# Performance work log

Measured on AMD Instinct MI355X. Metric: run time of the kernel, lower is better.

## Reference

```python
import jax, jax.numpy as jnp
import numpy as np

N = 50000
E = 400000
IN_DIM = 256
HID = 64
HEADS = 8
OUT_DIM = 40
NEG_SLOPE = 0.2  # PyG GATConv leaky-relu slope


def gat_conv(x, src, dst, W, a_src, a_dst, bias, concat):
    """One PyG-style GATConv (eval mode, self-loops already appended).
    x: [N, in], W: [in, H*C], a_src/a_dst: [H, C], bias: [H*C] or [C]."""
    H, C = a_src.shape
    h = (x @ W).reshape(N, H, C)                       # [N, H, C]
    # per-node attention logits, gathered per edge
    e_src = (h * a_src[None]).sum(-1)                  # [N, H]
    e_dst = (h * a_dst[None]).sum(-1)                  # [N, H]
    alpha = jax.nn.leaky_relu(e_src[src] + e_dst[dst], NEG_SLOPE)  # [Etot, H]
    # segment softmax over incoming edges of each dst node
    amax = jax.ops.segment_max(alpha, dst, num_segments=N)         # [N, H]
    ex = jnp.exp(alpha - amax[dst])
    denom = jax.ops.segment_sum(ex, dst, num_segments=N)           # [N, H]
    coef = ex / denom[dst]                                         # [Etot, H]
    # weighted scatter-add of neighbor features
    msg = h[src] * coef[:, :, None]                                # [Etot, H, C]
    out = jax.ops.segment_sum(msg, dst, num_segments=N)            # [N, H, C]
    out = out.reshape(N, H * C) if concat else out.mean(axis=1)
    return out + bias


def setup_inputs() -> dict:
    key = jax.random.key(0)
    ks = jax.random.split(key, 10)
    x = jax.random.normal(ks[0], (N, IN_DIM), dtype=jnp.float32)
    edge_index = jax.random.randint(ks[1], (2, E), 0, N, dtype=jnp.int32)
    g1 = 1.0 / np.sqrt(IN_DIM)
    g2 = 1.0 / np.sqrt(HID * HEADS)
    W1 = jax.random.normal(ks[2], (IN_DIM, HEADS * HID), dtype=jnp.float32) * g1
    a_src1 = jax.random.normal(ks[3], (HEADS, HID), dtype=jnp.float32) * 0.1
    a_dst1 = jax.random.normal(ks[4], (HEADS, HID), dtype=jnp.float32) * 0.1
    b1 = jnp.zeros((HEADS * HID,), dtype=jnp.float32)
    W2 = jax.random.normal(ks[5], (HEADS * HID, OUT_DIM), dtype=jnp.float32) * g2
    a_src2 = jax.random.normal(ks[6], (1, OUT_DIM), dtype=jnp.float32) * 0.1
    a_dst2 = jax.random.normal(ks[7], (1, OUT_DIM), dtype=jnp.float32) * 0.1
    b2 = jnp.zeros((OUT_DIM,), dtype=jnp.float32)
    return {"x": x, "edge_index": edge_index, "W1": W1, "a_src1": a_src1,
            "a_dst1": a_dst1, "b1": b1, "W2": W2, "a_src2": a_src2,
            "a_dst2": a_dst2, "b2": b2}


def reference(x, edge_index, W1, a_src1, a_dst1, b1, W2, a_src2, a_dst2, b2):
    # append self loops (PyG GATConv default add_self_loops=True)
    loop = jnp.arange(N, dtype=edge_index.dtype)
    src = jnp.concatenate([edge_index[0], loop])
    dst = jnp.concatenate([edge_index[1], loop])
    h = gat_conv(x, src, dst, W1, a_src1, a_dst1, b1, concat=True)
    h = jax.nn.elu(h)
    # dropout is identity in eval mode
    out = gat_conv(h, src, dst, W2, a_src2, a_dst2, b2, concat=False)
    return out
```

## Files before the change

kernel.cpp:

```cpp
#include <hip/hip_runtime.h>
#include <hip/hip_bf16.h>
#include <math.h>

#define IN_DIM 256
#define HEADS 8
#define HID 64
#define HC1 512
#define OUT_DIM 40
#define NEG_SLOPE 0.2f

typedef __attribute__((ext_vector_type(8))) short short8;
typedef __attribute__((ext_vector_type(4))) float f32x4;

__device__ __forceinline__ unsigned short f2b(float f) {
    __hip_bfloat16 h = __float2bfloat16(f);
    unsigned short u;
    __builtin_memcpy(&u, &h, 2);
    return u;
}

#define LRELU(a) ((a) > 0.f ? (a) : NEG_SLOPE * (a))

#define NB_W ((HC1 * IN_DIM + 48 * HC1 + 255) / 256)

__global__ __launch_bounds__(256) void prologue_kernel(
    const float* __restrict__ W1, const float* __restrict__ W2,
    __hip_bfloat16* __restrict__ W1T, __hip_bfloat16* __restrict__ W2T,
    const int* __restrict__ ei, int* __restrict__ deg, int E, int ET)
{
    int b = blockIdx.x;
    if (b < NB_W) {
        int i = b * 256 + threadIdx.x;
        if (i < HC1 * IN_DIM) {
            int n = i >> 8, k = i & 255;
            W1T[i] = __float2bfloat16(W1[(size_t)k * HC1 + n]);
        }
        int j = i - HC1 * IN_DIM;
        if (j >= 0 && j < 48 * HC1) {
            int n = j >> 9, k = j & 511;
            W2T[j] = __float2bfloat16(n < OUT_DIM ? W2[(size_t)k * OUT_DIM + n] : 0.f);
        }
    } else {
        int e = (b - NB_W) * 256 + threadIdx.x;
        if (e >= ET) return;
        int d = (e < E) ? ei[E + e] : e - E;
        atomicAdd(&deg[d], 1);
    }
}


__global__ __launch_bounds__(256) void scan1_kernel(
    const int* __restrict__ deg, int* __restrict__ rowptr,
    int* __restrict__ aux, int N)
{
    __shared__ int sd[256];
    int tid = threadIdx.x;
    int i = blockIdx.x * 256 + tid;
    int v = (i < N) ? deg[i] : 0;
    sd[tid] = v;
    __syncthreads();
    for (int off = 1; off < 256; off <<= 1) {
        int t = (tid >= off) ? sd[tid - off] : 0;
        __syncthreads();
        sd[tid] += t;
        __syncthreads();
    }
    if (i < N) rowptr[i] = sd[tid] - v;
    if (tid == 255) aux[blockIdx.x] = sd[255];
}

__global__ __launch_bounds__(256) void scan_aux_kernel(int* __restrict__ aux, int nb)
{
    __shared__ int sd[256];
    int tid = threadIdx.x;
    int v = (tid < nb) ? aux[tid] : 0;
    sd[tid] = v;
    __syncthreads();
    for (int off = 1; off < 256; off <<= 1) {
        int t = (tid >= off) ? sd[tid - off] : 0;
        __syncthreads();
        sd[tid] += t;
        __syncthreads();
    }
    if (tid < nb) aux[tid] = sd[tid] - v;
}

__global__ __launch_bounds__(256) void scan_add_kernel(
    int* __restrict__ rowptr, int* __restrict__ cursor,
    const int* __restrict__ aux, int N, int ET)
{
    int i = blockIdx.x * 256 + threadIdx.x;
    if (i < N) {
        int v = rowptr[i] + aux[blockIdx.x];
        rowptr[i] = v;
        cursor[i] = v;
    }
    if (i == 0) rowptr[N] = ET;
}

__global__ __launch_bounds__(256) void build_kernel(
    const int* __restrict__ ei, int* __restrict__ cursor,
    int* __restrict__ csr_src, int E, int ET)
{
    int e = blockIdx.x * 256 + threadIdx.x;
    if (e >= ET) return;
    int s, d;
    if (e < E) { s = ei[e]; d = ei[E + e]; } else { s = d = e - E; }
    int pos = atomicAdd(&cursor[d], 1);
    csr_src[pos] = s;
}

__global__ __launch_bounds__(512) void gemm1_mfma(
    const float* __restrict__ x, const __hip_bfloat16* __restrict__ W1T,
    const float* __restrict__ a_src1, const float* __restrict__ a_dst1,
    __hip_bfloat16* __restrict__ h1, float* __restrict__ e_src1,
    float* __restrict__ e_dst1, int N)
{
    __shared__ __hip_bfloat16 As[64][264];
    const int tid = threadIdx.x;
    const int row0 = blockIdx.x * 64;

    {
        int rr = tid >> 3;
        int cb = (tid & 7) * 32;
        int rowc = row0 + rr; if (rowc >= N) rowc = N - 1;
        const float* xp = x + (size_t)rowc * IN_DIM + cb;
#pragma unroll
        for (int j = 0; j < 4; ++j) {
            float4 a0 = *(const float4*)(xp + 8 * j);
            float4 a1 = *(const float4*)(xp + 8 * j + 4);
            short8 v;
            v[0] = f2b(a0.x); v[1] = f2b(a0.y); v[2] = f2b(a0.z); v[3] = f2b(a0.w);
            v[4] = f2b(a1.x); v[5] = f2b(a1.y); v[6] = f2b(a1.z); v[7] = f2b(a1.w);
            *(short8*)(&As[rr][cb + 8 * j]) = v;
        }
    }
    __syncthreads();

    const int w = tid >> 6;
    const int lane = tid & 63;
    const int r = lane & 15, g = lane >> 4;

    f32x4 acc[4][4] = {};
    const short* bp = (const short*)W1T + (size_t)(w * 64 + r) * IN_DIM + 8 * g;

#pragma unroll 2
    for (int kk = 0; kk < IN_DIM; kk += 32) {
        short8 af[4];
#pragma unroll
        for (int rt = 0; rt < 4; ++rt)
            af[rt] = *(const short8*)(&As[rt * 16 + r][kk + 8 * g]);
        short8 bf[4];
#pragma unroll
        for (int t = 0; t < 4; ++t)
            bf[t] = *(const short8*)(bp + (size_t)t * 16 * IN_DIM + kk);
#pragma unroll
        for (int t = 0; t < 4; ++t)
#pragma unroll
            for (int rt = 0; rt < 4; ++rt)
                acc[rt][t] = __builtin_amdgcn_mfma_f32_16x16x32_bf16(
                    af[rt], bf[t], acc[rt][t], 0, 0, 0);
    }

#pragma unroll
    for (int rt = 0; rt < 4; ++rt)
#pragma unroll
        for (int t = 0; t < 4; ++t) {
            int c = w * 64 + t * 16 + r;
#pragma unroll
            for (int q = 0; q < 4; ++q) {
                int row = row0 + rt * 16 + 4 * g + q;
                if (row < N)
                    h1[(size_t)row * HC1 + c] = __float2bfloat16(acc[rt][t][q]);
            }
        }

    float a1v[4], a2v[4];
#pragma unroll
    for (int t = 0; t < 4; ++t) {
        a1v[t] = a_src1[w * 64 + t * 16 + r];
        a2v[t] = a_dst1[w * 64 + t * 16 + r];
    }
#pragma unroll
    for (int rt = 0; rt < 4; ++rt) {
        float ps[4] = {}, pd[4] = {};
#pragma unroll
        for (int t = 0; t < 4; ++t)
#pragma unroll
            for (int q = 0; q < 4; ++q) {
                ps[q] += acc[rt][t][q] * a1v[t];
                pd[q] += acc[rt][t][q] * a2v[t];
            }
#pragma unroll
        for (int off = 1; off < 16; off <<= 1)
#pragma unroll
            for (int q = 0; q < 4; ++q) {
                ps[q] += __shfl_xor(ps[q], off);
                pd[q] += __shfl_xor(pd[q], off);
            }
        if (r == 0) {
#pragma unroll
            for (int q = 0; q < 4; ++q) {
                int row = row0 + rt * 16 + 4 * g + q;
                if (row < N) {
                    e_src1[row * 8 + w] = ps[q];
                    e_dst1[row * 8 + w] = pd[q];
                }
            }
        }
    }
}

__global__ __launch_bounds__(256) void gather1_kernel(
    const int* __restrict__ rowptr, const int* __restrict__ csr_src,
    const __hip_bfloat16* __restrict__ h1, const float* __restrict__ e_src,
    const float* __restrict__ e_dst, const float* __restrict__ b1,
    __hip_bfloat16* __restrict__ hmid, int N)
{
    int d = blockIdx.x * 4 + (threadIdx.x >> 6);
    if (d >= N) return;
    const int lane = threadIdx.x & 63;
    const int h0 = lane >> 3;
    const int base = rowptr[d];
    const int deg = rowptr[d + 1] - base;
    const float edv = e_dst[d * 8 + (lane & 7)];

    float acc[8] = {};
    float ssum = 0.f;

    const int nch = (deg + 7) >> 3;
    for (int c = 0; c < nch; ++c) {
        int i = c * 8 + (lane >> 3);
        int ii = i < deg ? i : deg - 1;
        int s = csr_src[base + ii];
        float v = e_src[s * 8 + (lane & 7)] + edv;
        float coef = (i < deg) ? __expf(LRELU(v)) : 0.f;

        uint4 u[8];
        float ce[8];
#pragma unroll
        for (int e = 0; e < 8; ++e) {
            ce[e] = __shfl(coef, e * 8 + h0);
            int se = __shfl(s, e * 8);
            u[e] = *(const uint4*)(h1 + (size_t)se * HC1 + 8 * lane);
        }
#pragma unroll
        for (int e = 0; e < 8; ++e) {
            acc[0] += ce[e] * __uint_as_float(u[e].x << 16);
            acc[1] += ce[e] * __uint_as_float(u[e].x & 0xffff0000u);
            acc[2] += ce[e] * __uint_as_float(u[e].y << 16);
            acc[3] += ce[e] * __uint_as_float(u[e].y & 0xffff0000u);
            acc[4] += ce[e] * __uint_as_float(u[e].z << 16);
            acc[5] += ce[e] * __uint_as_float(u[e].z & 0xffff0000u);
            acc[6] += ce[e] * __uint_as_float(u[e].w << 16);
            acc[7] += ce[e] * __uint_as_float(u[e].w & 0xffff0000u);
            ssum += ce[e];
        }
    }

    float inv = 1.f / ssum;
    float4 b0 = *(const float4*)(b1 + 8 * lane);
    float4 b4 = *(const float4*)(b1 + 8 * lane + 4);
    float ob[8];
    ob[0] = acc[0] * inv + b0.x; ob[1] = acc[1] * inv + b0.y;
    ob[2] = acc[2] * inv + b0.z; ob[3] = acc[3] * inv + b0.w;
    ob[4] = acc[4] * inv + b4.x; ob[5] = acc[5] * inv + b4.y;
    ob[6] = acc[6] * inv + b4.z; ob[7] = acc[7] * inv + b4.w;
    unsigned short rr[8];
#pragma unroll
    for (int j = 0; j < 8; ++j) {
        float o = ob[j];
        o = o > 0.f ? o : expm1f(o);
        rr[j] = f2b(o);
    }
    *(uint4*)(hmid + (size_t)d * HC1 + 8 * lane) = *(uint4*)rr;
}

__global__ __launch_bounds__(256) void gemm2_mfma(
    const __hip_bfloat16* __restrict__ hmid, const __hip_bfloat16* __restrict__ W2T,
    const float* __restrict__ a_src2, const float* __restrict__ a_dst2,
    float* __restrict__ h2, float* __restrict__ e_src2, float* __restrict__ e_dst2,
    int N)
{
    __shared__ __hip_bfloat16 Bs[48][520];
    const int tid = threadIdx.x;

    {
        const short* wp = (const short*)W2T;
#pragma unroll
        for (int i = 0; i < 12; ++i) {
            int idx = tid + i * 256;
            int row = idx >> 6, ch = idx & 63;
            *(short8*)(&Bs[row][ch * 8]) = *(const short8*)(wp + (size_t)row * HC1 + ch * 8);
        }
    }
    __syncthreads();

    const int w = tid >> 6;
    const int lane = tid & 63;
    const int r = lane & 15, g = lane >> 4;
    const int rowW = blockIdx.x * 64 + w * 16;

    int arow = rowW + r; if (arow >= N) arow = N - 1;
    const short* ap = (const short*)hmid + (size_t)arow * HC1 + 8 * g;

    f32x4 acc[3] = {};
#pragma unroll 4
    for (int kk = 0; kk < HC1; kk += 32) {
        short8 af = *(const short8*)(ap + kk);
        short8 bf[3];
#pragma unroll
        for (int t = 0; t < 3; ++t)
            bf[t] = *(const short8*)(&Bs[t * 16 + r][kk + 8 * g]);
#pragma unroll
        for (int t = 0; t < 3; ++t)
            acc[t] = __builtin_amdgcn_mfma_f32_16x16x32_bf16(af, bf[t], acc[t], 0, 0, 0);
    }

#pragma unroll
    for (int t = 0; t < 3; ++t) {
        int c = t * 16 + r;
        if (c < OUT_DIM) {
#pragma unroll
            for (int q = 0; q < 4; ++q) {
                int row = rowW + 4 * g + q;
                if (row < N) h2[(size_t)row * OUT_DIM + c] = acc[t][q];
            }
        }
    }

    float as[3], ad[3];
#pragma unroll
    for (int t = 0; t < 3; ++t) {
        int c = t * 16 + r;
        as[t] = (c < OUT_DIM) ? a_src2[c] : 0.f;
        ad[t] = (c < OUT_DIM) ? a_dst2[c] : 0.f;
    }
    float ps[4] = {}, pd[4] = {};
#pragma unroll
    for (int t = 0; t < 3; ++t)
#pragma unroll
        for (int q = 0; q < 4; ++q) {
            ps[q] += acc[t][q] * as[t];
            pd[q] += acc[t][q] * ad[t];
        }
#pragma unroll
    for (int off = 1; off < 16; off <<= 1)
#pragma unroll
        for (int q = 0; q < 4; ++q) {
            ps[q] += __shfl_xor(ps[q], off);
            pd[q] += __shfl_xor(pd[q], off);
        }
    if (r == 0) {
#pragma unroll
        for (int q = 0; q < 4; ++q) {
            int row = rowW + 4 * g + q;
            if (row < N) { e_src2[row] = ps[q]; e_dst2[row] = pd[q]; }
        }
    }
}

__global__ __launch_bounds__(256) void gather2_kernel(
    const int* __restrict__ rowptr, const int* __restrict__ csr_src,
    const float* __restrict__ h2, const float* __restrict__ e_src,
    const float* __restrict__ e_dst, const float* __restrict__ b2,
    float* __restrict__ out, int N)
{
    int wid = (blockIdx.x * blockDim.x + threadIdx.x) >> 6;
    if (wid >= N) return;
    int lane = threadIdx.x & 63;
    int base = rowptr[wid], end = rowptr[wid + 1];
    float ed = e_dst[wid];
    bool act = lane < OUT_DIM;
    int ln = act ? lane : 0;

    float acc = 0.f, ssum = 0.f;
    int j = base;
    for (; j + 4 <= end; j += 4) {
        int s0 = csr_src[j], s1 = csr_src[j + 1], s2 = csr_src[j + 2], s3 = csr_src[j + 3];
        float v0 = e_src[s0] + ed, v1 = e_src[s1] + ed;
        float v2 = e_src[s2] + ed, v3 = e_src[s3] + ed;
        float f0 = h2[(size_t)s0 * OUT_DIM + ln];
        float f1 = h2[(size_t)s1 * OUT_DIM + ln];
        float f2 = h2[(size_t)s2 * OUT_DIM + ln];
        float f3 = h2[(size_t)s3 * OUT_DIM + ln];
        float e0 = __expf(LRELU(v0)), e1 = __expf(LRELU(v1));
        float e2 = __expf(LRELU(v2)), e3 = __expf(LRELU(v3));
        acc += e0 * f0 + e1 * f1 + e2 * f2 + e3 * f3;
        ssum += e0 + e1 + e2 + e3;
    }
    for (; j < end; ++j) {
        int s0 = csr_src[j];
        float v0 = e_src[s0] + ed;
        float f0 = h2[(size_t)s0 * OUT_DIM + ln];
        float e0 = __expf(LRELU(v0));
        acc += e0 * f0;
        ssum += e0;
    }
    if (act)
        out[(size_t)wid * OUT_DIM + lane] = acc / ssum + b2[lane];
}

extern "C" void kernel_launch(void* const* d_in, const int* in_sizes, int n_in,
                              void* d_out, int out_size, void* d_ws, size_t ws_size,
                              hipStream_t stream)
{
    const float* x      = (const float*)d_in[0];
    const int*   ei     = (const int*)d_in[1];
    const float* W1     = (const float*)d_in[2];
    const float* a_src1 = (const float*)d_in[3];
    const float* a_dst1 = (const float*)d_in[4];
    const float* b1     = (const float*)d_in[5];
    const float* W2     = (const float*)d_in[6];
    const float* a_src2 = (const float*)d_in[7];
    const float* a_dst2 = (const float*)d_in[8];
    const float* b2     = (const float*)d_in[9];
    float* out = (float*)d_out;

    const int N  = in_sizes[0] / IN_DIM;
    const int E  = in_sizes[1] / 2;
    const int ET = E + N;

    char* p = (char*)d_ws;
    auto alloc = [&](size_t bytes) -> void* {
        void* r = (void*)p;
        p += (bytes + 255) & ~(size_t)255;
        return r;
    };
    __hip_bfloat16* h1b    = (__hip_bfloat16*)alloc((size_t)N * HC1 * 2);
    __hip_bfloat16* hmid   = (__hip_bfloat16*)alloc((size_t)N * HC1 * 2);
    float*    h2      = (float*)alloc((size_t)N * OUT_DIM * 4);
    float*    e_src1  = (float*)alloc((size_t)N * HEADS * 4);
    float*    e_dst1  = (float*)alloc((size_t)N * HEADS * 4);
    float*    e_src2  = (float*)alloc((size_t)N * 4);
    float*    e_dst2  = (float*)alloc((size_t)N * 4);
    int*      deg     = (int*)alloc((size_t)N * 4);
    int*      rowptr  = (int*)alloc((size_t)(N + 1) * 4);
    int*      cursor  = (int*)alloc((size_t)N * 4);
    int*      csr_src = (int*)alloc((size_t)ET * 4);
    int*      aux     = (int*)alloc(256 * 4);
    __hip_bfloat16* W1T = (__hip_bfloat16*)alloc((size_t)HC1 * IN_DIM * 2);
    __hip_bfloat16* W2T = (__hip_bfloat16*)alloc((size_t)48 * HC1 * 2);

    const int nbN  = (N + 255) / 256;
    const int nbET = (ET + 255) / 256;

    hipMemsetAsync(deg, 0, (size_t)N * 4, stream);
    prologue_kernel<<<NB_W + nbET, 256, 0, stream>>>(W1, W2, W1T, W2T, ei, deg, E, ET);

    scan1_kernel<<<nbN, 256, 0, stream>>>(deg, rowptr, aux, N);
    scan_aux_kernel<<<1, 256, 0, stream>>>(aux, nbN);
    scan_add_kernel<<<nbN, 256, 0, stream>>>(rowptr, cursor, aux, N, ET);
    build_kernel<<<nbET, 256, 0, stream>>>(ei, cursor, csr_src, E, ET);

    gemm1_mfma<<<(N + 63) / 64, 512, 0, stream>>>(x, W1T, a_src1, a_dst1, h1b,
                                                  e_src1, e_dst1, N);
    gather1_kernel<<<(N + 3) / 4, 256, 0, stream>>>(rowptr, csr_src, h1b, e_src1,
                                                    e_dst1, b1, hmid, N);

    gemm2_mfma<<<(N + 63) / 64, 256, 0, stream>>>(hmid, W2T, a_src2, a_dst2, h2,
                                                  e_src2, e_dst2, N);
    gather2_kernel<<<(N + 3) / 4, 256, 0, stream>>>(rowptr, csr_src, h2, e_src2,
                                                    e_dst2, b2, out, N);
}
```

Before: 235.1 us.

## Merge scan kernels, preload GEMM operands into registers, trim gather tail

```diff
diff --git a/kernel.cpp b/kernel.cpp
--- a/kernel.cpp
+++ b/kernel.cpp
@@ -69,29 +69,23 @@
     if (tid == 255) aux[blockIdx.x] = sd[255];
 }
 
-__global__ __launch_bounds__(256) void scan_aux_kernel(int* __restrict__ aux, int nb)
+__global__ __launch_bounds__(256) void scan_finish_kernel(
+    int* __restrict__ rowptr, int* __restrict__ cursor,
+    const int* __restrict__ aux, int N, int ET)
 {
     __shared__ int sd[256];
     int tid = threadIdx.x;
-    int v = (tid < nb) ? aux[tid] : 0;
-    sd[tid] = v;
+    sd[tid] = (tid < blockIdx.x) ? aux[tid] : 0;
     __syncthreads();
-    for (int off = 1; off < 256; off <<= 1) {
-        int t = (tid >= off) ? sd[tid - off] : 0;
+#pragma unroll
+    for (int off = 128; off > 0; off >>= 1) {
+        if (tid < off) sd[tid] += sd[tid + off];
         __syncthreads();
-        sd[tid] += t;
-        __syncthreads();
-    }
-    if (tid < nb) aux[tid] = sd[tid] - v;
-}
-
-__global__ __launch_bounds__(256) void scan_add_kernel(
-    int* __restrict__ rowptr, int* __restrict__ cursor,
-    const int* __restrict__ aux, int N, int ET)
-{
-    int i = blockIdx.x * 256 + threadIdx.x;
+    }
+    int prefix = sd[0];
+    int i = blockIdx.x * 256 + tid;
     if (i < N) {
-        int v = rowptr[i] + aux[blockIdx.x];
+        int v = rowptr[i] + prefix;
         rowptr[i] = v;
         cursor[i] = v;
     }
@@ -119,6 +113,17 @@
     __shared__ __hip_bfloat16 As[64][264];
     const int tid = threadIdx.x;
     const int row0 = blockIdx.x * 64;
+    const int w = tid >> 6;
+    const int lane = tid & 63;
+    const int r = lane & 15, g = lane >> 4;
+
+    const short* bp = (const short*)W1T + (size_t)(w * 64 + r) * IN_DIM + 8 * g;
+    short8 breg[8][4];
+#pragma unroll
+    for (int k8 = 0; k8 < 8; ++k8)
+#pragma unroll
+        for (int t = 0; t < 4; ++t)
+            breg[k8][t] = *(const short8*)(bp + (size_t)t * 16 * IN_DIM + k8 * 32);
 
     {
         int rr = tid >> 3;
@@ -137,29 +142,19 @@
     }
     __syncthreads();
 
-    const int w = tid >> 6;
-    const int lane = tid & 63;
-    const int r = lane & 15, g = lane >> 4;
-
     f32x4 acc[4][4] = {};
-    const short* bp = (const short*)W1T + (size_t)(w * 64 + r) * IN_DIM + 8 * g;
-
-#pragma unroll 2
-    for (int kk = 0; kk < IN_DIM; kk += 32) {
+#pragma unroll
+    for (int k8 = 0; k8 < 8; ++k8) {
         short8 af[4];
 #pragma unroll
         for (int rt = 0; rt < 4; ++rt)
-            af[rt] = *(const short8*)(&As[rt * 16 + r][kk + 8 * g]);
-        short8 bf[4];
-#pragma unroll
-        for (int t = 0; t < 4; ++t)
-            bf[t] = *(const short8*)(bp + (size_t)t * 16 * IN_DIM + kk);
+            af[rt] = *(const short8*)(&As[rt * 16 + r][k8 * 32 + 8 * g]);
 #pragma unroll
         for (int t = 0; t < 4; ++t)
 #pragma unroll
             for (int rt = 0; rt < 4; ++rt)
                 acc[rt][t] = __builtin_amdgcn_mfma_f32_16x16x32_bf16(
-                    af[rt], bf[t], acc[rt][t], 0, 0, 0);
+                    af[rt], breg[k8][t], acc[rt][t], 0, 0, 0);
     }
 
 #pragma unroll
@@ -236,25 +231,20 @@
         float v = e_src[s * 8 + (lane & 7)] + edv;
         float coef = (i < deg) ? __expf(LRELU(v)) : 0.f;
 
-        uint4 u[8];
-        float ce[8];
-#pragma unroll
-        for (int e = 0; e < 8; ++e) {
-            ce[e] = __shfl(coef, e * 8 + h0);
+        int emax = deg - c * 8; if (emax > 8) emax = 8;
+        for (int e = 0; e < emax; ++e) {
+            float ce = __shfl(coef, e * 8 + h0);
             int se = __shfl(s, e * 8);
-            u[e] = *(const uint4*)(h1 + (size_t)se * HC1 + 8 * lane);
-        }
-#pragma unroll
-        for (int e = 0; e < 8; ++e) {
-            acc[0] += ce[e] * __uint_as_float(u[e].x << 16);
-            acc[1] += ce[e] * __uint_as_float(u[e].x & 0xffff0000u);
-            acc[2] += ce[e] * __uint_as_float(u[e].y << 16);
-            acc[3] += ce[e] * __uint_as_float(u[e].y & 0xffff0000u);
-            acc[4] += ce[e] * __uint_as_float(u[e].z << 16);
-            acc[5] += ce[e] * __uint_as_float(u[e].z & 0xffff0000u);
-            acc[6] += ce[e] * __uint_as_float(u[e].w << 16);
-            acc[7] += ce[e] * __uint_as_float(u[e].w & 0xffff0000u);
-            ssum += ce[e];
+            uint4 u = *(const uint4*)(h1 + ((size_t)se << 9) + 8 * lane);
+            acc[0] += ce * __uint_as_float(u.x << 16);
+            acc[1] += ce * __uint_as_float(u.x & 0xffff0000u);
+            acc[2] += ce * __uint_as_float(u.y << 16);
+            acc[3] += ce * __uint_as_float(u.y & 0xffff0000u);
+            acc[4] += ce * __uint_as_float(u.z << 16);
+            acc[5] += ce * __uint_as_float(u.z & 0xffff0000u);
+            acc[6] += ce * __uint_as_float(u.w << 16);
+            acc[7] += ce * __uint_as_float(u.w & 0xffff0000u);
+            ssum += ce;
         }
     }
 
@@ -284,6 +274,17 @@
 {
     __shared__ __hip_bfloat16 Bs[48][520];
     const int tid = threadIdx.x;
+    const int w = tid >> 6;
+    const int lane = tid & 63;
+    const int r = lane & 15, g = lane >> 4;
+    const int rowW = blockIdx.x * 64 + w * 16;
+
+    int arow = rowW + r; if (arow >= N) arow = N - 1;
+    const short* ap = (const short*)hmid + (size_t)arow * HC1 + 8 * g;
+    short8 areg[16];
+#pragma unroll
+    for (int kk = 0; kk < 16; ++kk)
+        areg[kk] = *(const short8*)(ap + kk * 32);
 
     {
         const short* wp = (const short*)W2T;
@@ -296,25 +297,16 @@
     }
     __syncthreads();
 
-    const int w = tid >> 6;
-    const int lane = tid & 63;
-    const int r = lane & 15, g = lane >> 4;
-    const int rowW = blockIdx.x * 64 + w * 16;
-
-    int arow = rowW + r; if (arow >= N) arow = N - 1;
-    const short* ap = (const short*)hmid + (size_t)arow * HC1 + 8 * g;
-
     f32x4 acc[3] = {};
-#pragma unroll 4
-    for (int kk = 0; kk < HC1; kk += 32) {
-        short8 af = *(const short8*)(ap + kk);
+#pragma unroll
+    for (int kk = 0; kk < 16; ++kk) {
         short8 bf[3];
 #pragma unroll
         for (int t = 0; t < 3; ++t)
-            bf[t] = *(const short8*)(&Bs[t * 16 + r][kk + 8 * g]);
+            bf[t] = *(const short8*)(&Bs[t * 16 + r][kk * 32 + 8 * g]);
 #pragma unroll
         for (int t = 0; t < 3; ++t)
-            acc[t] = __builtin_amdgcn_mfma_f32_16x16x32_bf16(af, bf[t], acc[t], 0, 0, 0);
+            acc[t] = __builtin_amdgcn_mfma_f32_16x16x32_bf16(areg[kk], bf[t], acc[t], 0, 0, 0);
     }
 
 #pragma unroll
@@ -449,8 +441,7 @@
     prologue_kernel<<<NB_W + nbET, 256, 0, stream>>>(W1, W2, W1T, W2T, ei, deg, E, ET);
 
     scan1_kernel<<<nbN, 256, 0, stream>>>(deg, rowptr, aux, N);
-    scan_aux_kernel<<<1, 256, 0, stream>>>(aux, nbN);
-    scan_add_kernel<<<nbN, 256, 0, stream>>>(rowptr, cursor, aux, N, ET);
+    scan_finish_kernel<<<nbN, 256, 0, stream>>>(rowptr, cursor, aux, N, ET);
     build_kernel<<<nbET, 256, 0, stream>>>(ei, cursor, csr_src, E, ET);
 
     gemm1_mfma<<<(N + 63) / 64, 512, 0, stream>>>(x, W1T, a_src1, a_dst1, h1b,
```

Result: no change. 238.9 us (+1.6%).
